# Performance work log

Hardware: AMD Instinct MI355X
Metric: run time of the kernel (lower is better)

Reference implementation:

```python
import jax, jax.numpy as jnp
import numpy as np

IN_F, OUT_F = 4096, 4096
GROUP = 128
N_GROUPS = IN_F // GROUP
R, NUM_A, NUM_B = 16, 2, 2
LORA_ALPHA = 32
SCALING = LORA_ALPHA / R  # 2.0
BITS = 4
PACK = 32 // BITS  # 8 int4 per int32


def dequant_gptq(qweight, qzeros, scales, g_idx):
    """Unpack int4 GPTQ weights -> dense [in_features, out_features] fp32."""
    shifts = (jnp.arange(PACK, dtype=jnp.int32) * BITS)
    # qweight: [in/8, out] packed along in dim
    wq = (qweight[:, None, :] >> shifts[None, :, None]) & 0xF       # [in/8, 8, out]
    wq = wq.reshape(IN_F, OUT_F).astype(jnp.float32)
    # qzeros: [n_groups, out/8] packed along out dim
    zq = (qzeros[:, :, None] >> shifts[None, None, :]) & 0xF        # [g, out/8, 8]
    zq = zq.reshape(N_GROUPS, OUT_F).astype(jnp.float32)
    # per-row group lookup
    return scales[g_idx] * (wq - zq[g_idx])                          # [in, out]


def activation_weights(x, normalize=True):
    # 'inps' mode: per-input-feature importance from mean |activation|
    w = jnp.mean(jnp.abs(x), axis=tuple(range(x.ndim - 1)))          # [in]
    if normalize:
        w = w / (jnp.mean(w) + 1e-6)
    return w


def setup_inputs() -> dict:
    key = jax.random.key(0)
    ks = jax.random.split(key, 8)
    x = jax.random.normal(ks[0], (2, 2048, IN_F), dtype=jnp.float32)
    scales = jax.random.uniform(ks[1], (N_GROUPS, OUT_F), dtype=jnp.float32) * 0.01 + 0.001
    bias = jax.random.normal(ks[2], (OUT_F,), dtype=jnp.float32) * 0.01
    lora_A = jax.random.normal(ks[3], (NUM_A, R, IN_F), dtype=jnp.float32) * (1.0 / np.sqrt(IN_F))
    lora_B = jax.random.normal(ks[4], (NUM_B, OUT_F, R), dtype=jnp.float32) * 0.01
    qweight = jax.random.randint(ks[5], (IN_F // PACK, OUT_F), 0, 2147483647, dtype=jnp.int32)
    qzeros = jax.random.randint(ks[6], (N_GROUPS, OUT_F // PACK), 0, 2147483647, dtype=jnp.int32)
    g_idx = (jnp.arange(IN_F, dtype=jnp.int32) // GROUP).astype(jnp.int32)
    return {"x": x, "scales": scales, "bias": bias, "lora_A": lora_A,
            "lora_B": lora_B, "qweight": qweight, "qzeros": qzeros, "g_idx": g_idx}


def reference(x, scales, bias, lora_A, lora_B, qweight, qzeros, g_idx):
    W = dequant_gptq(qweight, qzeros, scales, g_idx)                 # [in, out]
    result = jnp.einsum('bsi,io->bso', x, W) + bias                  # base GPTQ linear
    # activation-aware 'inps' weighting (dropout p=0 -> identity, eval mode)
    aw = activation_weights(x, normalize=True)                       # [in]
    x_w = x * aw                                                     # broadcast on last dim
    # sum_{i,j} B_j(A_i(x_w)) == (sum_j B_j) @ (sum_i A_i) @ x_w (all linear, no bias)
    A_sum = jnp.sum(lora_A, axis=0)                                  # [r, in]
    B_sum = jnp.sum(lora_B, axis=0)                                  # [out, r]
    h = jnp.einsum('bsi,ri->bsr', x_w, A_sum)                        # [b, s, r]
    result = result + jnp.einsum('bsr,or->bso', h, B_sum) * SCALING
    return result
```

## Files before the change

kernel.cpp:

```cpp
#include <hip/hip_runtime.h>
#include <stdint.h>

#define IN_F 4096
#define OUT_F 4096

typedef __attribute__((ext_vector_type(4))) float f32x4;
typedef __attribute__((ext_vector_type(16))) float f32x16;
typedef _Float16 f16x8 __attribute__((ext_vector_type(8)));
typedef _Float16 f16x2 __attribute__((ext_vector_type(2)));
typedef unsigned short u16x8 __attribute__((ext_vector_type(8)));

__device__ __forceinline__ unsigned short f2h(float f) {
  _Float16 h = (_Float16)f;
  return __builtin_bit_cast(unsigned short, h);
}

#define SIGMA_TAB 0x73625140u

#define OFF_XH     ((size_t)0)
#define OFF_PART   ((size_t)33554432)
#define OFF_W      ((size_t)35651584)
#define OFF_BSUM   ((size_t)35667968)
#define OFF_AW     ((size_t)35668480)
#define OFF_BS     ((size_t)35799552)
#define OFF_HPART  ((size_t)36061696)
#define OFF_HB     ((size_t)38158848)
#define WS_NEED    ((size_t)38420992)

__global__ __launch_bounds__(256) void k1_prep(const float* __restrict__ x,
                                               unsigned short* __restrict__ xh,
                                               float* __restrict__ part) {
  int t = threadIdx.x;
  int c8 = (blockIdx.x * 256 + t) * 8;
  int by = blockIdx.y;
  float a[8];
  #pragma unroll
  for (int i = 0; i < 8; ++i) a[i] = 0.f;
  for (int rr = 0; rr < 32; ++rr) {
    size_t off = (size_t)(by * 32 + rr) * IN_F + c8;
    f32x4 v0 = *(const f32x4*)(x + off);
    f32x4 v1 = *(const f32x4*)(x + off + 4);
    u16x8 o;
    o[0] = f2h(v0[0]); o[1] = f2h(v1[0]); o[2] = f2h(v0[1]); o[3] = f2h(v1[1]);
    o[4] = f2h(v0[2]); o[5] = f2h(v1[2]); o[6] = f2h(v0[3]); o[7] = f2h(v1[3]);
    *(u16x8*)(xh + off) = o;
    a[0] += fabsf(v0[0]); a[1] += fabsf(v0[1]); a[2] += fabsf(v0[2]); a[3] += fabsf(v0[3]);
    a[4] += fabsf(v1[0]); a[5] += fabsf(v1[1]); a[6] += fabsf(v1[2]); a[7] += fabsf(v1[3]);
  }
  f32x4 p0 = { a[0], a[1], a[2], a[3] };
  f32x4 p1 = { a[4], a[5], a[6], a[7] };
  *(f32x4*)(part + (size_t)by * IN_F + c8) = p0;
  *(f32x4*)(part + (size_t)by * IN_F + c8 + 4) = p1;
}

__global__ __launch_bounds__(256) void k2_colred(const float* __restrict__ part,
                                                 float* __restrict__ w,
                                                 float* __restrict__ bsum) {
  int t = threadIdx.x;
  int col = blockIdx.x * 256 + t;
  float s = 0.f;
  for (int st = 0; st < 128; ++st) s += part[(size_t)st * IN_F + col];
  float wv = s * (1.0f / 4096.0f);
  w[col] = wv;
  __shared__ float red[256];
  red[t] = wv; __syncthreads();
  for (int k = 128; k > 0; k >>= 1) { if (t < k) red[t] += red[t + k]; __syncthreads(); }
  if (t == 0) bsum[blockIdx.x] = red[0];
}

__global__ __launch_bounds__(256) void k3_fold(const float* __restrict__ lora_A,
                                               const float* __restrict__ lora_B,
                                               const float* __restrict__ w,
                                               const float* __restrict__ bsum,
                                               unsigned short* __restrict__ A_w,
                                               unsigned short* __restrict__ Bs) {
  int b = blockIdx.x, t = threadIdx.x;
  float s = 0.f;
  #pragma unroll
  for (int i = 0; i < 16; ++i) s += bsum[i];
  float iv = 1.0f / (s * (1.0f / 4096.0f) + 1e-6f);
  if (b < 256) {
    int idx = b * 256 + t;
    int r = idx >> 12;
    int pos = idx & 4095;
    int p = pos & 7;
    int orig = (pos & ~7) + (int)((SIGMA_TAB >> (p * 4)) & 7);
    float v = (lora_A[(size_t)r * IN_F + orig] + lora_A[(size_t)(16 + r) * IN_F + orig]) * w[orig] * iv;
    A_w[idx] = f2h(v);
  } else {
    int idx = (b - 256) * 256 + t;
    int o = idx >> 5, r = idx & 31;
    float v = 0.f;
    if (r < 16) v = 2.0f * (lora_B[o * 16 + r] + lora_B[OUT_F * 16 + o * 16 + r]);
    Bs[idx] = f2h(v);
  }
}

__global__ __launch_bounds__(256) void k4_h(const unsigned short* __restrict__ xh,
                                            const unsigned short* __restrict__ A_w,
                                            float* __restrict__ hpart) {
  int mb = blockIdx.x, kc = blockIdx.y;
  int t = threadIdx.x, wid = t >> 6, l = t & 63;
  int m0 = mb * 128 + wid * 32;
  int lr = l & 15, lg = l >> 4;
  f32x4 z = { 0.f, 0.f, 0.f, 0.f };
  f32x4 acc0 = z, acc1 = z;
  for (int it = 0; it < 16; ++it) {
    int k = kc * 512 + it * 32 + lg * 8;
    f16x8 b  = *(const f16x8*)(A_w + (size_t)lr * IN_F + k);
    f16x8 a0 = *(const f16x8*)(xh + (size_t)(m0 + lr) * IN_F + k);
    f16x8 a1 = *(const f16x8*)(xh + (size_t)(m0 + 16 + lr) * IN_F + k);
    acc0 = __builtin_amdgcn_mfma_f32_16x16x32_f16(a0, b, acc0, 0, 0, 0);
    acc1 = __builtin_amdgcn_mfma_f32_16x16x32_f16(a1, b, acc1, 0, 0, 0);
  }
  float* hp = hpart + (size_t)kc * IN_F * 16;
  #pragma unroll
  for (int r = 0; r < 4; ++r) {
    hp[(size_t)(m0 + lg * 4 + r) * 16 + lr]      = acc0[r];
    hp[(size_t)(m0 + 16 + lg * 4 + r) * 16 + lr] = acc1[r];
  }
}

__global__ __launch_bounds__(256) void k5_hred(const float* __restrict__ hpart,
                                               unsigned short* __restrict__ hb) {
  int gid = blockIdx.x * 256 + threadIdx.x;
  int m = gid >> 5, r = gid & 31;
  float v = 0.f;
  if (r < 16)
    for (int kc = 0; kc < 8; ++kc) v += hpart[(size_t)kc * 65536 + m * 16 + r];
  hb[gid] = f2h(v);
}

__device__ __forceinline__ f16x8 deq8(unsigned int q, f16x2 s2, f16x2 zz2) {
  unsigned int u0 = ( q         & 0x000F000Fu) | 0x64006400u;
  unsigned int u1 = ((q >> 4)   & 0x000F000Fu) | 0x64006400u;
  unsigned int u2 = ((q >> 8)   & 0x000F000Fu) | 0x64006400u;
  unsigned int u3 = ((q >> 12)  & 0x000F000Fu) | 0x64006400u;
  f16x2 w0 = (__builtin_bit_cast(f16x2, u0) - zz2) * s2;
  f16x2 w1 = (__builtin_bit_cast(f16x2, u1) - zz2) * s2;
  f16x2 w2 = (__builtin_bit_cast(f16x2, u2) - zz2) * s2;
  f16x2 w3 = (__builtin_bit_cast(f16x2, u3) - zz2) * s2;
  struct { f16x2 a, b, c, d; } r { w0, w1, w2, w3 };
  return __builtin_bit_cast(f16x8, r);
}

__global__ __launch_bounds__(256) void k6_gemm(const unsigned short* __restrict__ xh,
                                               const int* __restrict__ qweight,
                                               const int* __restrict__ qzeros,
                                               const float* __restrict__ scales,
                                               const float* __restrict__ bias,
                                               const unsigned short* __restrict__ hb,
                                               const unsigned short* __restrict__ Bs,
                                               float* __restrict__ out) {
  __shared__ __align__(16) unsigned short As[2][128 * 128];
  int t = threadIdx.x, w = t >> 6, l = t & 63;
  int lr = l & 15;
  int lc = l & 31;
  int hi = l >> 5;
  int b0 = blockIdx.x;
  int bid = (b0 & 7) * 128 + (b0 >> 3);
  int mt = bid >> 5, nt = bid & 31;
  int m0 = mt * 128, n0 = nt * 128;
  int ncol = n0 + w * 32 + lc;

  f32x16 acc[4];
  #pragma unroll
  for (int m = 0; m < 4; ++m)
    #pragma unroll
    for (int r = 0; r < 16; ++r) acc[m][r] = 0.f;

  int row0 = t >> 4;
  int cp = (t & 15) ^ row0;
  const unsigned short* aE = xh + (size_t)(m0 + row0) * IN_F + cp * 8;
  const int*   qE = qweight + (size_t)hi * OUT_F + ncol;
  const float* sE = scales + ncol;
  const int*   zE = qzeros + (ncol >> 3);
  int zsh = (l & 7) * 4;

  #define STAGE_A(BUF, APTR) do {                                                 \
    _Pragma("unroll")                                                             \
    for (int it = 0; it < 8; ++it) {                                              \
      const unsigned short* gp = (APTR) + (size_t)it * 16 * IN_F;                 \
      __builtin_amdgcn_global_load_lds((const __attribute__((address_space(1))) void*)gp, \
                                       (__attribute__((address_space(3))) void*)(&As[BUF][0] + (it * 256 + t) * 8), \
                                       16, 0, 0);                                 \
    }                                                                             \
  } while (0)

  #define LOAD_QW(QW, QPTR) do {                                                  \
    _Pragma("unroll")                                                             \
    for (int ks = 0; ks < 8; ++ks)                                                \
      QW[ks] = (unsigned int)(QPTR)[ks * 2 * OUT_F];                              \
  } while (0)

  #define LOAD_CONST(S2, ZP, SPTR, ZPTR) do {                                     \
    float s_ = (SPTR)[0];                                                         \
    unsigned int zi = (unsigned int)(ZPTR)[0];                                    \
    unsigned int z = (zi >> zsh) & 0xFu;                                          \
    unsigned int zzu = 0x64006400u + z * 0x00010001u;                             \
    ZP = __builtin_bit_cast(f16x2, zzu);                                          \
    _Float16 sh = (_Float16)s_;                                                   \
    unsigned int sb = (unsigned int)__builtin_bit_cast(unsigned short, sh);       \
    unsigned int ssu = (sb << 16) | sb;                                           \
    S2 = __builtin_bit_cast(f16x2, ssu);                                          \
  } while (0)

  #define COMPUTE(BUF, QW, S2, ZP) do {                                           \
    _Pragma("unroll")                                                             \
    for (int ks = 0; ks < 8; ++ks) {                                              \
      f16x8 bf = deq8(QW[ks], S2, ZP);                                            \
      int chunk_ = (ks * 2 + hi) ^ lr;                                            \
      f16x8 a[4];                                                                 \
      _Pragma("unroll")                                                           \
      for (int m = 0; m < 4; ++m)                                                 \
        a[m] = *(const f16x8*)(&As[BUF][0] + (m * 32 + lc) * 128 + chunk_ * 8);   \
      __builtin_amdgcn_s_setprio(1);                                              \
      _Pragma("unroll")                                                           \
      for (int m = 0; m < 4; ++m)                                                 \
        acc[m] = __builtin_amdgcn_mfma_f32_32x32x16_f16(a[m], bf, acc[m], 0, 0, 0); \
      __builtin_amdgcn_s_setprio(0);                                              \
    }                                                                             \
  } while (0)

  unsigned int qwA[8], qwB[8];
  f16x2 s2a, zpa, s2b, zpb;

  STAGE_A(0, aE);
  LOAD_QW(qwA, qE);
  LOAD_CONST(s2a, zpa, sE, zE);
  const unsigned short* aO = aE + 128;
  const int*   qO = qE + 16 * OUT_F;
  const float* sO = sE + OUT_F;
  const int*   zO = zE + OUT_F / 8;
  aE += 256; qE += 32 * OUT_F; sE += 2 * OUT_F; zE += 2 * (OUT_F / 8);
  __syncthreads();

  for (int kt = 0; kt < 32; kt += 2) {
    LOAD_QW(qwB, qO);
    LOAD_CONST(s2b, zpb, sO, zO);
    STAGE_A(1, aO);
    COMPUTE(0, qwA, s2a, zpa);
    __syncthreads();
    if (kt + 2 < 32) {
      LOAD_QW(qwA, qE);
      LOAD_CONST(s2a, zpa, sE, zE);
      STAGE_A(0, aE);
    }
    COMPUTE(1, qwB, s2b, zpb);
    __syncthreads();
    aO += 256; qO += 32 * OUT_F; sO += 2 * OUT_F; zO += 2 * (OUT_F / 8);
    aE += 256; qE += 32 * OUT_F; sE += 2 * OUT_F; zE += 2 * (OUT_F / 8);
  }
  #undef STAGE_A
  #undef LOAD_QW
  #undef LOAD_CONST
  #undef COMPUTE

  {
    f16x8 bb = *(const f16x8*)(Bs + (size_t)ncol * 32 + hi * 8);
    #pragma unroll
    for (int m = 0; m < 4; ++m) {
      f16x8 ah = *(const f16x8*)(hb + (size_t)(m0 + m * 32 + lc) * 32 + hi * 8);
      acc[m] = __builtin_amdgcn_mfma_f32_32x32x16_f16(ah, bb, acc[m], 0, 0, 0);
    }
  }
  {
    float bv = bias[ncol];
    #pragma unroll
    for (int m = 0; m < 4; ++m) {
      int rbase = m0 + m * 32 + 4 * hi;
      #pragma unroll
      for (int r = 0; r < 16; ++r) {
        int orow = rbase + (r & 3) + 8 * (r >> 2);
        out[(size_t)orow * OUT_F + ncol] = acc[m][r] + bv;
      }
    }
  }
}

extern "C" void kernel_launch(void* const* d_in, const int* in_sizes, int n_in,
                              void* d_out, int out_size, void* d_ws, size_t ws_size,
                              hipStream_t stream) {
  const float* x       = (const float*)d_in[0];
  const float* scales  = (const float*)d_in[1];
  const float* bias    = (const float*)d_in[2];
  const float* lora_A  = (const float*)d_in[3];
  const float* lora_B  = (const float*)d_in[4];
  const int*   qweight = (const int*)d_in[5];
  const int*   qzeros  = (const int*)d_in[6];
  float* out = (float*)d_out;

  if (ws_size < WS_NEED) return;

  char* ws = (char*)d_ws;
  unsigned short* xh  = (unsigned short*)(ws + OFF_XH);
  float* part         = (float*)(ws + OFF_PART);
  float* w            = (float*)(ws + OFF_W);
  float* bsum         = (float*)(ws + OFF_BSUM);
  unsigned short* A_w = (unsigned short*)(ws + OFF_AW);
  unsigned short* Bs  = (unsigned short*)(ws + OFF_BS);
  float* hpart        = (float*)(ws + OFF_HPART);
  unsigned short* hb  = (unsigned short*)(ws + OFF_HB);

  k1_prep<<<dim3(2, 128), 256, 0, stream>>>(x, xh, part);
  k2_colred<<<16, 256, 0, stream>>>(part, w, bsum);
  k3_fold<<<768, 256, 0, stream>>>(lora_A, lora_B, w, bsum, A_w, Bs);
  k4_h<<<dim3(32, 8), 256, 0, stream>>>(xh, A_w, hpart);
  k5_hred<<<512, 256, 0, stream>>>(hpart, hb);
  k6_gemm<<<1024, 256, 0, stream>>>(xh, qweight, qzeros, scales, bias, hb, Bs, out);
}
```

Before: 187.9 us.

## Halve GEMM K-tile to 64 and raise occupancy with a new LDS swizzle

The K tile of the fused dequant GEMM shrinks from 128 to 64. LDS per block halves to 32KB, and launch bounds now request 4 blocks per CU for more occupancy and latency hiding. A new XOR swizzle matches the 64-wide rows, and the per-group scale and zero loads are now fetched once per group of two K-tiles. The cost is twice as many loop iterations and barriers, plus possible register pressure from the occupancy hint.

```diff
diff --git a/kernel.cpp b/kernel.cpp
--- a/kernel.cpp
+++ b/kernel.cpp
@@ -144,21 +144,20 @@
   return __builtin_bit_cast(f16x8, r);
 }
 
-__global__ __launch_bounds__(256) void k6_gemm(const unsigned short* __restrict__ xh,
-                                               const int* __restrict__ qweight,
-                                               const int* __restrict__ qzeros,
-                                               const float* __restrict__ scales,
-                                               const float* __restrict__ bias,
-                                               const unsigned short* __restrict__ hb,
-                                               const unsigned short* __restrict__ Bs,
-                                               float* __restrict__ out) {
-  __shared__ __align__(16) unsigned short As[2][128 * 128];
+__global__ __launch_bounds__(256, 4) void k6_gemm(const unsigned short* __restrict__ xh,
+                                                  const int* __restrict__ qweight,
+                                                  const int* __restrict__ qzeros,
+                                                  const float* __restrict__ scales,
+                                                  const float* __restrict__ bias,
+                                                  const unsigned short* __restrict__ hb,
+                                                  const unsigned short* __restrict__ Bs,
+                                                  float* __restrict__ out) {
+  __shared__ __align__(16) unsigned short As[2][128 * 64];
   int t = threadIdx.x, w = t >> 6, l = t & 63;
-  int lr = l & 15;
   int lc = l & 31;
   int hi = l >> 5;
-  int b0 = blockIdx.x;
-  int bid = (b0 & 7) * 128 + (b0 >> 3);
+  int b0id = blockIdx.x;
+  int bid = (b0id & 7) * 128 + (b0id >> 3);
   int mt = bid >> 5, nt = bid & 31;
   int m0 = mt * 128, n0 = nt * 128;
   int ncol = n0 + w * 32 + lc;
@@ -169,18 +168,21 @@
     #pragma unroll
     for (int r = 0; r < 16; ++r) acc[m][r] = 0.f;
 
-  int row0 = t >> 4;
-  int cp = (t & 15) ^ row0;
-  const unsigned short* aE = xh + (size_t)(m0 + row0) * IN_F + cp * 8;
+  int row0 = t >> 3;
+  int cpA = (t & 7) ^ ((row0 + w) & 7);
+  int cpB = cpA ^ 4;
+  const unsigned short* aE = xh + (size_t)(m0 + row0) * IN_F;
   const int*   qE = qweight + (size_t)hi * OUT_F + ncol;
-  const float* sE = scales + ncol;
-  const int*   zE = qzeros + (ncol >> 3);
+  const float* sC = scales + ncol;
+  const int*   zC = qzeros + (ncol >> 3);
   int zsh = (l & 7) * 4;
+  int fbase = (lc + (lc >> 3)) & 7;
 
   #define STAGE_A(BUF, APTR) do {                                                 \
     _Pragma("unroll")                                                             \
-    for (int it = 0; it < 8; ++it) {                                              \
-      const unsigned short* gp = (APTR) + (size_t)it * 16 * IN_F;                 \
+    for (int it = 0; it < 4; ++it) {                                              \
+      int cp_ = (it & 1) ? cpB : cpA;                                             \
+      const unsigned short* gp = (APTR) + (size_t)it * 32 * IN_F + cp_ * 8;       \
       __builtin_amdgcn_global_load_lds((const __attribute__((address_space(1))) void*)gp, \
                                        (__attribute__((address_space(3))) void*)(&As[BUF][0] + (it * 256 + t) * 8), \
                                        16, 0, 0);                                 \
@@ -189,7 +191,7 @@
 
   #define LOAD_QW(QW, QPTR) do {                                                  \
     _Pragma("unroll")                                                             \
-    for (int ks = 0; ks < 8; ++ks)                                                \
+    for (int ks = 0; ks < 4; ++ks)                                                \
       QW[ks] = (unsigned int)(QPTR)[ks * 2 * OUT_F];                              \
   } while (0)
 
@@ -207,13 +209,15 @@
 
   #define COMPUTE(BUF, QW, S2, ZP) do {                                           \
     _Pragma("unroll")                                                             \
-    for (int ks = 0; ks < 8; ++ks) {                                              \
+    for (int ks = 0; ks < 4; ++ks) {                                              \
       f16x8 bf = deq8(QW[ks], S2, ZP);                                            \
-      int chunk_ = (ks * 2 + hi) ^ lr;                                            \
+      int lch = ks * 2 + hi;                                                      \
       f16x8 a[4];                                                                 \
       _Pragma("unroll")                                                           \
-      for (int m = 0; m < 4; ++m)                                                 \
-        a[m] = *(const f16x8*)(&As[BUF][0] + (m * 32 + lc) * 128 + chunk_ * 8);   \
+      for (int m = 0; m < 4; ++m) {                                               \
+        int chunk = lch ^ ((fbase + 4 * m) & 7);                                  \
+        a[m] = *(const f16x8*)(&As[BUF][0] + (m * 32 + lc) * 64 + chunk * 8);     \
+      }                                                                           \
       __builtin_amdgcn_s_setprio(1);                                              \
       _Pragma("unroll")                                                           \
       for (int m = 0; m < 4; ++m)                                                 \
@@ -222,34 +226,34 @@
     }                                                                             \
   } while (0)
 
-  unsigned int qwA[8], qwB[8];
-  f16x2 s2a, zpa, s2b, zpb;
+  unsigned int qwA[4], qwB[4];
+  f16x2 s2a, zpa, s2n, zpn;
 
   STAGE_A(0, aE);
   LOAD_QW(qwA, qE);
-  LOAD_CONST(s2a, zpa, sE, zE);
-  const unsigned short* aO = aE + 128;
-  const int*   qO = qE + 16 * OUT_F;
-  const float* sO = sE + OUT_F;
-  const int*   zO = zE + OUT_F / 8;
-  aE += 256; qE += 32 * OUT_F; sE += 2 * OUT_F; zE += 2 * (OUT_F / 8);
+  LOAD_CONST(s2a, zpa, sC, zC);
+  sC += OUT_F; zC += OUT_F / 8;
+  const unsigned short* aO = aE + 64;
+  const int*   qO = qE + 8 * OUT_F;
+  aE += 128; qE += 16 * OUT_F;
   __syncthreads();
 
-  for (int kt = 0; kt < 32; kt += 2) {
+  for (int kt = 0; kt < 64; kt += 2) {
     LOAD_QW(qwB, qO);
-    LOAD_CONST(s2b, zpb, sO, zO);
     STAGE_A(1, aO);
     COMPUTE(0, qwA, s2a, zpa);
     __syncthreads();
-    if (kt + 2 < 32) {
+    if (kt + 2 < 64) {
       LOAD_QW(qwA, qE);
-      LOAD_CONST(s2a, zpa, sE, zE);
+      LOAD_CONST(s2n, zpn, sC, zC);
       STAGE_A(0, aE);
     }
-    COMPUTE(1, qwB, s2b, zpb);
+    COMPUTE(1, qwB, s2a, zpa);
     __syncthreads();
-    aO += 256; qO += 32 * OUT_F; sO += 2 * OUT_F; zO += 2 * (OUT_F / 8);
-    aE += 256; qE += 32 * OUT_F; sE += 2 * OUT_F; zE += 2 * (OUT_F / 8);
+    s2a = s2n; zpa = zpn;
+    sC += OUT_F; zC += OUT_F / 8;
+    aO += 128; qO += 16 * OUT_F;
+    aE += 128; qE += 16 * OUT_F;
   }
   #undef STAGE_A
   #undef LOAD_QW
```

Result: slower. 193.7 us (+3.1%).
